# Performance work log

Hardware: AMD Instinct MI355X
Metric: run time of the kernel (lower is better)

## Reference

```python
import jax, jax.numpy as jnp
import numpy as np

N = 8192      # nodes
E = 131072    # global edges
SDIM = 256    # scalar channels
VDIM = 64     # vector channels
EDIM = 128    # edge feature dim
L = 5         # num_layers
DIN = 2 * SDIM + EDIM + 4        # [s_src, s_tgt, e, d, a, |p_src|, |p_tgt|]
DOUT = SDIM + 2 * VDIM + 1 + EDIM  # [m_s, w_v1, w_v2, w_p, e_new]
HID = SDIM


def setup_inputs() -> dict:
    key = jax.random.key(0)
    ks = jax.random.split(key, 12)
    s = jax.random.normal(ks[0], (N, SDIM), jnp.float32)
    v = 0.1 * jax.random.normal(ks[1], (N, 3, VDIM), jnp.float32)
    p = 3.0 * jax.random.normal(ks[2], (N, 3), jnp.float32)
    e = jax.random.normal(ks[3], (E, EDIM), jnp.float32)
    edge_index = jax.random.randint(ks[4], (2, E), 0, N, dtype=jnp.int32)
    W1 = jax.random.normal(ks[5], (L, DIN, HID), jnp.float32) / np.sqrt(DIN)
    W2 = jax.random.normal(ks[6], (L, HID, DOUT), jnp.float32) / np.sqrt(HID)
    U1 = jax.random.normal(ks[7], (L, SDIM, SDIM), jnp.float32) / np.sqrt(SDIM)
    U2 = jax.random.normal(ks[8], (L, SDIM, SDIM), jnp.float32) / np.sqrt(SDIM)
    return {
        's': s, 'v': v, 'p': p, 'e': e, 'edge_index': edge_index,
        'ln_g': jnp.ones((L, SDIM), jnp.float32),
        'ln_b': jnp.zeros((L, SDIM), jnp.float32),
        'W1': W1, 'b1': jnp.zeros((L, HID), jnp.float32),
        'W2': W2, 'b2': jnp.zeros((L, DOUT), jnp.float32),
        'U1': U1, 'bU1': jnp.zeros((L, SDIM), jnp.float32),
        'U2': U2, 'bU2': jnp.zeros((L, SDIM), jnp.float32),
    }


def _edge_attrs(edge_index, pos):
    # Faithful to calculate_edge_attrs (sqrt=True, no ligand-pocket branch)
    src, tgt = edge_index[0], edge_index[1]
    r = pos[tgt] - pos[src]                                   # [E,3]
    a = jnp.sum(pos[tgt] * pos[src], axis=-1)                 # [E]
    d = jnp.sqrt(jnp.clip(jnp.sum(r * r, axis=-1), 1e-6, None))
    r_norm = r / (1.0 + d[:, None])
    return d, a, r_norm


def reference(s, v, p, e, edge_index, ln_g, ln_b, W1, b1, W2, b2, U1, bU1, U2, bU2):
    src, tgt = edge_index[0], edge_index[1]
    d, a, rn = _edge_attrs(edge_index, p)
    # in-degree counts for 'mean' vector/position aggregation
    cnt = jnp.clip(jax.ops.segment_sum(jnp.ones((E,), s.dtype), tgt, num_segments=N), 1.0)
    for i in range(L):
        # LayerNorm on scalar channels (vectors passed through)
        mu = jnp.mean(s, axis=-1, keepdims=True)
        var = jnp.mean((s - mu) ** 2, axis=-1, keepdims=True)
        s_ln = ln_g[i] * (s - mu) * jax.lax.rsqrt(var + 1e-5) + ln_b[i]
        pn = jnp.linalg.norm(p, axis=-1, keepdims=True)       # use_pos_norm features
        # gather-compute edge messages
        feat = jnp.concatenate(
            [s_ln[src], s_ln[tgt], e, d[:, None], a[:, None], pn[src], pn[tgt]], axis=-1)
        h = jax.nn.silu(feat @ W1[i] + b1[i])                 # [E,HID]
        out = h @ W2[i] + b2[i]                               # [E,DOUT]
        m_s = out[:, :SDIM]
        wv1 = out[:, SDIM:SDIM + VDIM]
        wv2 = out[:, SDIM + VDIM:SDIM + 2 * VDIM]
        wp = out[:, SDIM + 2 * VDIM:SDIM + 2 * VDIM + 1]
        e_new = out[:, SDIM + 2 * VDIM + 1:]
        has_v = 0.0 if i == 0 else 1.0                        # has_v_in = (i > 0)
        m_v = has_v * wv1[:, None, :] * v[src] + wv2[:, None, :] * rn[:, :, None]  # [E,3,VDIM]
        m_p = jnp.tanh(wp) * rn                               # [E,3]
        # scatter-aggregate (sum for scalars, mean for vectors/positions)
        s = s + jax.ops.segment_sum(m_s, tgt, num_segments=N)
        v = v + jax.ops.segment_sum(m_v, tgt, num_segments=N) / cnt[:, None, None]
        p = p + jax.ops.segment_sum(m_p, tgt, num_segments=N) / cnt[:, None]
        if i < L - 1:                                         # use_mlp_update = (i < num_layers - 1)
            s = s + jax.nn.silu(s @ U1[i] + bU1[i]) @ U2[i] + bU2[i]
        e = jax.nn.silu(e_new)
        # recompute_edge_attributes=True: redo gather/distance math on new positions
        d, a, rn = _edge_attrs(edge_index, p)
    return s, v, e, p
```

## Files before the change

### kernel.cpp

```cpp
#include <hip/hip_runtime.h>
#include <hip/hip_bf16.h>

namespace {

constexpr int NN   = 8192;
constexpr int NE   = 131072;
constexpr int SD   = 256;
constexpr int ED   = 128;
constexpr int NL   = 5;
constexpr int DINc = 644;
constexpr int KE   = 160;
constexpr int TE   = 5;
constexpr int T2   = 8;
constexpr int DOUTc= 513;
constexpr int HIDc = 256;

typedef __bf16 bf16x8 __attribute__((ext_vector_type(8)));
typedef float  f32x4  __attribute__((ext_vector_type(4)));

__device__ __forceinline__ float siluf(float x) { return x / (1.0f + __expf(-x)); }

__device__ __forceinline__ void gl_lds16(const void* gsrc, void* lds_uniform_base) {
  __builtin_amdgcn_global_load_lds(
      (const __attribute__((address_space(1))) unsigned int*)gsrc,
      (__attribute__((address_space(3))) unsigned int*)lds_uniform_base, 16, 0, 0);
}

__device__ __forceinline__ void wait_vm4() {
  asm volatile("s_waitcnt vmcnt(4)" ::: "memory");
  __builtin_amdgcn_sched_barrier(0);
}
__device__ __forceinline__ void wait_vm0() {
  asm volatile("s_waitcnt vmcnt(0)" ::: "memory");
  __builtin_amdgcn_sched_barrier(0);
}

__device__ __host__ __forceinline__ int swz(int kc) { return (kc * 5) & 7; }
__device__ __forceinline__ int apos(int kc, int row) { return kc * 64  + (row ^ swz(kc)); }
__device__ __forceinline__ int bpos(int kc, int n)   { return kc * 256 + (n   ^ swz(kc)); }

enum { MODE_LIN = 4 };
enum { SRC_BF16 = 1, SRC_F32 = 2 };

struct GemmArgs {
  const __hip_bfloat16* Wt;
  const float* bias;
  const __hip_bfloat16* Abf;
  const float* Af32;
  __hip_bfloat16* bf_out;
  const __hip_bfloat16* Wtb;
  const float* biasb;
  __hip_bfloat16* bf_outb;
  int dual;
};

__device__ __forceinline__ uint4 cvt8f(const float* p) {
  alignas(16) __hip_bfloat16 t8[8];
#pragma unroll
  for (int i = 0; i < 8; i++) t8[i] = __float2bfloat16(p[i]);
  return *(const uint4*)t8;
}

template<int MODE, int SRC, int KTOT, int BM>
__global__ __launch_bounds__(256) void gemm_k(GemmArgs g) {
  constexpr int T = KTOT / 32;
  constexpr int NC = KTOT / 8;
  constexpr int RPT = 256 / BM;
  constexpr int RMASK = RPT - 1;
  __shared__ alignas(16) unsigned short Apan[NC * BM * 8];
  __shared__ alignas(16) unsigned short Bsh[2][4 * 256 * 8];
  const int tid = threadIdx.x, lane = tid & 63, wave = tid >> 6;
  const int l16 = lane & 15, lhi = lane >> 4;
  const __hip_bfloat16* wtp = g.Wt;
  const float* biasp = g.bias;
  __hip_bfloat16* outp = g.bf_out;
  int blk = blockIdx.x;
  {
    const int half = gridDim.x >> 1;
    if (g.dual && blk >= half) { blk -= half; wtp = g.Wtb; biasp = g.biasb; outp = g.bf_outb; }
  }
  const int row0 = blk * BM;
  const int ar = tid / RPT, aq = tid % RPT;
  const int arow = row0 + ar;
  f32x4 acc[BM / 16][4] = {};

  auto issueB = [&](int t, int buf) {
    const __hip_bfloat16* src = wtp + (size_t)t * 1024 * 8;
    unsigned short* dst = &Bsh[buf][0];
#pragma unroll
    for (int i = 0; i < 4; i++)
      gl_lds16(src + (size_t)(i * 256 + wave * 64 + lane) * 8, dst + (i * 256 + wave * 64) * 8);
  };

  issueB(0, 0);
#pragma unroll
  for (int j = 0; j < NC / RPT; j++) {
    const int c = j * RPT + aq;
    uint4 o;
    if constexpr (SRC == SRC_BF16) o = *(const uint4*)(g.Abf + (size_t)arow * KTOT + c * 8);
    else                           o = cvt8f(g.Af32 + (size_t)arow * KTOT + c * 8);
    *(uint4*)&Apan[(c * BM + (ar ^ swz(aq))) * 8] = o;
  }
  __syncthreads();

  int cur = 0;
  for (int t = 0; t < T; ++t) {
    if (t + 1 < T) { issueB(t + 1, cur ^ 1); wait_vm4(); }
    else           { wait_vm0(); }
    bf16x8 bfr[4];
#pragma unroll
    for (int f = 0; f < 4; f++)
      bfr[f] = *(const bf16x8*)&Bsh[cur][bpos(lhi, wave * 64 + f * 16 + l16) * 8];
#pragma unroll
    for (int fr = 0; fr < BM / 16; fr++) {
      const int kc = t * 4 + lhi;
      const bf16x8 afr = *(const bf16x8*)&Apan[(kc * BM + ((fr * 16 + l16) ^ swz(kc & RMASK))) * 8];
#pragma unroll
      for (int fc = 0; fc < 4; fc++)
        acc[fr][fc] = __builtin_amdgcn_mfma_f32_16x16x32_bf16(afr, bfr[fc], acc[fr][fc], 0, 0, 0);
    }
    cur ^= 1;
  }

#pragma unroll
  for (int fr = 0; fr < BM / 16; fr++) {
#pragma unroll
    for (int fc = 0; fc < 4; fc++) {
      const int n = wave * 64 + fc * 16 + l16;
#pragma unroll
      for (int r = 0; r < 4; r++) {
        const int row = row0 + fr * 16 + lhi * 4 + r;
        outp[(size_t)row * HIDc + n] = __float2bfloat16(acc[fr][fc][r] + biasp[n]);
      }
    }
  }
}

struct Node3Args {
  const __hip_bfloat16* W2a;
  const __hip_bfloat16* U1s;
  const __hip_bfloat16* U2s;
  const float* b2L;
  const float* bU1;
  const float* bU2;
  const float* Hagg;
  const int* rawcnt;
  float* s_out;
};

template<int LAST>
__global__ __launch_bounds__(256) void node3_k(Node3Args g) {
  constexpr int BM = 32, RPT = 8, NC = 32, T = 8;
  __shared__ alignas(16) unsigned short Apan[NC * BM * 8];
  __shared__ alignas(16) unsigned short Bsh[2][4 * 256 * 8];
  const int tid = threadIdx.x, lane = tid & 63, wave = tid >> 6;
  const int l16 = lane & 15, lhi = lane >> 4;
  const int row0 = blockIdx.x * BM;
  const int ar = tid >> 3, aq = tid & 7;

  auto issueB = [&](const __hip_bfloat16* W, int t, int buf) {
    const __hip_bfloat16* src = W + (size_t)t * 1024 * 8;
    unsigned short* dst = &Bsh[buf][0];
#pragma unroll
    for (int i = 0; i < 4; i++)
      gl_lds16(src + (size_t)(i * 256 + wave * 64 + lane) * 8, dst + (i * 256 + wave * 64) * 8);
  };

  f32x4 acc[4][2];
  auto kloop = [&](const __hip_bfloat16* W) {
#pragma unroll
    for (int i = 0; i < 4; i++)
#pragma unroll
      for (int j = 0; j < 2; j++) acc[i][j] = f32x4{0.f, 0.f, 0.f, 0.f};
    int cur = 0;
    for (int t = 0; t < T; ++t) {
      if (t + 1 < T) { issueB(W, t + 1, cur ^ 1); wait_vm4(); }
      else           { wait_vm0(); }
      bf16x8 wfr[4], afr[2];
#pragma unroll
      for (int f = 0; f < 4; f++)
        wfr[f] = *(const bf16x8*)&Bsh[cur][bpos(lhi, wave * 64 + f * 16 + l16) * 8];
#pragma unroll
      for (int f = 0; f < 2; f++) {
        const int kc = t * 4 + lhi;
        afr[f] = *(const bf16x8*)&Apan[(kc * BM + ((f * 16 + l16) ^ swz(kc & 7))) * 8];
      }
#pragma unroll
      for (int fr = 0; fr < 4; fr++)
#pragma unroll
        for (int fc = 0; fc < 2; fc++)
          acc[fr][fc] = __builtin_amdgcn_mfma_f32_16x16x32_bf16(wfr[fr], afr[fc], acc[fr][fc], 0, 0, 0);
      cur ^= 1;
    }
  };

  issueB(g.W2a, 0, 0);
#pragma unroll
  for (int j = 0; j < NC / RPT; j++) {
    const int c = j * RPT + aq;
    uint4 o = cvt8f(g.Hagg + (size_t)(row0 + ar) * SD + c * 8);
    *(uint4*)&Apan[(c * BM + (ar ^ swz(aq))) * 8] = o;
  }
  __syncthreads();

  kloop(g.W2a);
  __syncthreads();
  if constexpr (!LAST) issueB(g.U1s, 0, 0);

#pragma unroll
  for (int fr = 0; fr < 4; fr++) {
    const int nb = wave * 64 + fr * 16 + lhi * 4;
    const int kc = nb >> 3, off = nb & 7;
    const f32x4 b4 = *(const f32x4*)(g.b2L + nb);
#pragma unroll
    for (int fc = 0; fc < 2; fc++) {
      const int row = fc * 16 + l16;
      const float rc = (float)g.rawcnt[row0 + row];
      float* sp = g.s_out + (size_t)(row0 + row) * SD + nb;
      f32x4 sold = *(const f32x4*)sp;
      alignas(8) __hip_bfloat16 hb[4];
      f32x4 s1;
#pragma unroll
      for (int r = 0; r < 4; r++) {
        s1[r] = sold[r] + acc[fr][fc][r] + rc * b4[r];
        hb[r] = __float2bfloat16(s1[r]);
      }
      *(f32x4*)sp = s1;
      if constexpr (!LAST)
        *(uint2*)&Apan[(kc * BM + (row ^ swz(kc & 7))) * 8 + off] = *(const uint2*)hb;
    }
  }
  if constexpr (LAST) return;

  __syncthreads();

  kloop(g.U1s);
  __syncthreads();
  issueB(g.U2s, 0, 0);
#pragma unroll
  for (int fr = 0; fr < 4; fr++) {
    const int nb = wave * 64 + fr * 16 + lhi * 4;
    const int kc = nb >> 3, off = nb & 7;
    const f32x4 b4 = *(const f32x4*)(g.bU1 + nb);
#pragma unroll
    for (int fc = 0; fc < 2; fc++) {
      const int row = fc * 16 + l16;
      alignas(8) __hip_bfloat16 hb[4];
#pragma unroll
      for (int r = 0; r < 4; r++)
        hb[r] = __float2bfloat16(siluf(acc[fr][fc][r] + b4[r]));
      *(uint2*)&Apan[(kc * BM + (row ^ swz(kc & 7))) * 8 + off] = *(const uint2*)hb;
    }
  }
  __syncthreads();

  kloop(g.U2s);
#pragma unroll
  for (int fr = 0; fr < 4; fr++) {
    const int nb = wave * 64 + fr * 16 + lhi * 4;
    const f32x4 b4 = *(const f32x4*)(g.bU2 + nb);
#pragma unroll
    for (int fc = 0; fc < 2; fc++) {
      const int row = fc * 16 + l16;
      float* sp = g.s_out + (size_t)(row0 + row) * SD + nb;
      f32x4 s1 = *(const f32x4*)sp;
#pragma unroll
      for (int r = 0; r < 4; r++) s1[r] += acc[fr][fc][r] + b4[r];
      *(f32x4*)sp = s1;
    }
  }
}

struct FusedArgs {
  const __hip_bfloat16* W1e;
  const __hip_bfloat16* W2s;
  const float* b2L;
  const int* src; const int* tgt;
  const int* rank;
  const __hip_bfloat16* e_bf;
  const __hip_bfloat16* tail;
  const __hip_bfloat16* p1;
  const __hip_bfloat16* p2;
  const __hip_bfloat16* w384;
  const float* rn;
  float* mp;
  __hip_bfloat16* h_out;
  __hip_bfloat16* wv_out;
  __hip_bfloat16* e_bf_out;
  float* e_f32_out;
  int write_e_f32;
};

__global__ __launch_bounds__(256) void fused_k(FusedArgs g) {
  __shared__ alignas(16) unsigned short Ash[4 * 64 * 8];
  __shared__ alignas(16) unsigned short Bsh[2][4 * 256 * 8];
  __shared__ alignas(16) unsigned short Hsh[32 * 64 * 8];
  __shared__ float wps[4][64];
  __shared__ int Rk[64];
  const int tid = threadIdx.x, lane = tid & 63, wave = tid >> 6;
  const int l16 = lane & 15, lhi = lane >> 4;
  const int row0 = blockIdx.x * 64;
  const int ar = tid >> 2, aq = tid & 3;
  const int arow = row0 + ar;
  const int sn = g.src[arow], tn = g.tgt[arow];

  auto issueW = [&](const __hip_bfloat16* W, int t, int buf) {
    const __hip_bfloat16* src = W + (size_t)t * 1024 * 8;
    unsigned short* dst = &Bsh[buf][0];
#pragma unroll
    for (int i = 0; i < 4; i++)
      gl_lds16(src + (size_t)(i * 256 + wave * 64 + lane) * 8, dst + (i * 256 + wave * 64) * 8);
  };
  auto loadA = [&](int t, uint4& o) {
    const int kq = t * 32 + aq * 8;
    if (kq < 128) o = *(const uint4*)(g.e_bf + (size_t)arow * ED + kq);
    else          o = *(const uint4*)(g.tail + (size_t)arow * 32 + (kq - 128));
  };

  uint4 a;
  loadA(0, a);
  issueW(g.W1e, 0, 0);
  if (tid < 64) Rk[tid] = g.rank[row0 + tid];

#pragma unroll
  for (int j = 0; j < 8; j++) {
    const int c = j * 4 + aq;
    uint4 r1 = *(const uint4*)(g.p1 + (size_t)sn * SD + c * 8);
    uint4 r2 = *(const uint4*)(g.p2 + (size_t)tn * SD + c * 8);
    const __hip_bfloat16* h1 = (const __hip_bfloat16*)&r1;
    const __hip_bfloat16* h2 = (const __hip_bfloat16*)&r2;
    alignas(16) __hip_bfloat16 o8[8];
#pragma unroll
    for (int m = 0; m < 8; m++)
      o8[m] = __float2bfloat16(__bfloat162float(h1[m]) + __bfloat162float(h2[m]));
    *(uint4*)&Hsh[(c * 64 + (ar ^ swz(aq))) * 8] = *(const uint4*)o8;
  }

  f32x4 acc1[4][4] = {};
  int cur = 0;
  for (int t = 0; t < TE; ++t) {
    *(uint4*)&Ash[apos(aq, ar) * 8] = a;
    __syncthreads();
    if (t + 1 < TE) { issueW(g.W1e, t + 1, cur ^ 1); loadA(t + 1, a); }
    bf16x8 wfr[4], efr[4];
#pragma unroll
    for (int f = 0; f < 4; f++) {
      wfr[f] = *(const bf16x8*)&Bsh[cur][bpos(lhi, wave * 64 + f * 16 + l16) * 8];
      efr[f] = *(const bf16x8*)&Ash[apos(lhi, f * 16 + l16) * 8];
    }
#pragma unroll
    for (int fr = 0; fr < 4; fr++)
#pragma unroll
      for (int fc = 0; fc < 4; fc++)
        acc1[fr][fc] = __builtin_amdgcn_mfma_f32_16x16x32_bf16(wfr[fr], efr[fc], acc1[fr][fc], 0, 0, 0);
    __syncthreads();
    cur ^= 1;
  }

  issueW(g.W2s, 0, 0);

  float pw[4] = {0.f, 0.f, 0.f, 0.f};
#pragma unroll
  for (int fr = 0; fr < 4; fr++) {
    const int nb = wave * 64 + fr * 16 + lhi * 4;
    const int kc = nb >> 3, off = nb & 7;
    uint2 wr = *(const uint2*)(g.w384 + nb);
    const __hip_bfloat16* w4 = (const __hip_bfloat16*)&wr;
#pragma unroll
    for (int fc = 0; fc < 4; fc++) {
      const int row = fc * 16 + l16;
      unsigned short* slot = &Hsh[(kc * 64 + (row ^ swz(kc & 3))) * 8 + off];
      uint2 pr = *(const uint2*)slot;
      const __hip_bfloat16* pp = (const __hip_bfloat16*)&pr;
      alignas(8) __hip_bfloat16 hb[4];
#pragma unroll
      for (int r = 0; r < 4; r++) {
        const float hv = siluf(acc1[fr][fc][r] + __bfloat162float(pp[r]));
        hb[r] = __float2bfloat16(hv);
        pw[fc] += hv * __bfloat162float(w4[r]);
      }
      *(uint2*)slot = *(const uint2*)hb;
      *(uint2*)(g.h_out + (size_t)Rk[row] * HIDc + nb) = *(const uint2*)hb;
    }
  }

#pragma unroll
  for (int fc = 0; fc < 4; fc++) {
    pw[fc] += __shfl_xor(pw[fc], 16);
    pw[fc] += __shfl_xor(pw[fc], 32);
  }
  if (lane < 16) {
#pragma unroll
    for (int fc = 0; fc < 4; fc++) wps[wave][fc * 16 + lane] = pw[fc];
  }
  __syncthreads();
  if (tid < 64) {
    const float s = wps[0][tid] + wps[1][tid] + wps[2][tid] + wps[3][tid];
    const float wpt = tanhf(s + g.b2L[384]);
    const int rk = Rk[tid];
#pragma unroll
    for (int c = 0; c < 3; c++)
      g.mp[(size_t)rk * 3 + c] = wpt * g.rn[(size_t)(row0 + tid) * 3 + c];
  }

  f32x4 acc2[4][4] = {};
  cur = 0;
  for (int t = 0; t < T2; ++t) {
    if (t + 1 < T2) { issueW(g.W2s, t + 1, cur ^ 1); wait_vm4(); }
    else            { wait_vm0(); }
    bf16x8 afr[4], bfr[4];
#pragma unroll
    for (int f = 0; f < 4; f++) {
      const int kc = t * 4 + lhi;
      afr[f] = *(const bf16x8*)&Hsh[(kc * 64 + ((f * 16 + l16) ^ swz(lhi))) * 8];
      bfr[f] = *(const bf16x8*)&Bsh[cur][bpos(lhi, wave * 64 + f * 16 + l16) * 8];
    }
#pragma unroll
    for (int fr = 0; fr < 4; fr++)
#pragma unroll
      for (int fc = 0; fc < 4; fc++)
        acc2[fr][fc] = __builtin_amdgcn_mfma_f32_16x16x32_bf16(afr[fr], bfr[fc], acc2[fr][fc], 0, 0, 0);
    cur ^= 1;
  }

#pragma unroll
  for (int fr = 0; fr < 4; fr++) {
#pragma unroll
    for (int fc = 0; fc < 4; fc++) {
      const int n = wave * 64 + fc * 16 + l16;
#pragma unroll
      for (int r = 0; r < 4; r++) {
        const int lr = fr * 16 + lhi * 4 + r;
        const int row = row0 + lr;
        const float valf = acc2[fr][fc][r];
        if (n < 128) {
          g.wv_out[(size_t)Rk[lr] * 128 + n] = __float2bfloat16(valf + g.b2L[256 + n]);
        } else {
          const float sv = siluf(valf + g.b2L[257 + n]);
          g.e_bf_out[(size_t)row * ED + (n - 128)] = __float2bfloat16(sv);
          if (g.write_e_f32) g.e_f32_out[(size_t)row * ED + (n - 128)] = sv;
        }
      }
    }
  }
}

__global__ __launch_bounds__(256) void ln_k(const float* __restrict__ s,
                                            const float* __restrict__ gl, const float* __restrict__ bl,
                                            __hip_bfloat16* __restrict__ s_ln) {
  const int wave = threadIdx.x >> 6, lane = threadIdx.x & 63;
  const int node = blockIdx.x * 4 + wave;
  const float* srow = s + (size_t)node * SD;
  float x[4], sum = 0.f, sq = 0.f;
#pragma unroll
  for (int i = 0; i < 4; i++) { x[i] = srow[lane * 4 + i]; sum += x[i]; sq += x[i] * x[i]; }
#pragma unroll
  for (int off = 1; off < 64; off <<= 1) { sum += __shfl_xor(sum, off); sq += __shfl_xor(sq, off); }
  const float mu = sum * (1.0f / SD);
  const float var = sq * (1.0f / SD) - mu * mu;
  const float rstd = rsqrtf(var + 1e-5f);
#pragma unroll
  for (int i = 0; i < 4; i++) {
    const int c = lane * 4 + i;
    s_ln[(size_t)node * SD + c] = __float2bfloat16(gl[c] * (x[i] - mu) * rstd + bl[c]);
  }
}

__global__ void edge_attr_k(const float* __restrict__ p, const int* __restrict__ src, const int* __restrict__ tgt,
                            const int* __restrict__ rank,
                            float* __restrict__ rn, float* __restrict__ rnp,
                            __hip_bfloat16* __restrict__ tail) {
  const int e = blockIdx.x * blockDim.x + threadIdx.x;
  if (e >= NE) return;
  const int s_ = src[e], t_ = tgt[e];
  const float sx = p[s_ * 3], sy = p[s_ * 3 + 1], sz = p[s_ * 3 + 2];
  const float tx = p[t_ * 3], ty = p[t_ * 3 + 1], tz = p[t_ * 3 + 2];
  const float rx = tx - sx, ry = ty - sy, rz = tz - sz;
  const float a = tx * sx + ty * sy + tz * sz;
  const float rr = rx * rx + ry * ry + rz * rz;
  const float d = sqrtf(fmaxf(rr, 1e-6f));
  const float inv = 1.0f / (1.0f + d);
  const float r0 = rx * inv, r1 = ry * inv, r2 = rz * inv;
  rn[e * 3] = r0; rn[e * 3 + 1] = r1; rn[e * 3 + 2] = r2;
  const int rk = rank[e];
  rnp[rk * 3] = r0; rnp[rk * 3 + 1] = r1; rnp[rk * 3 + 2] = r2;
  alignas(16) __hip_bfloat16 t8[8];
  t8[0] = __float2bfloat16(d);
  t8[1] = __float2bfloat16(a);
  t8[2] = __float2bfloat16(sqrtf(sx * sx + sy * sy + sz * sz));
  t8[3] = __float2bfloat16(sqrtf(tx * tx + ty * ty + tz * tz));
  t8[4] = t8[5] = t8[6] = t8[7] = __float2bfloat16(0.0f);
  __hip_bfloat16* tp = tail + (size_t)e * 32;
  uint4 z; z.x = z.y = z.z = z.w = 0;
  *(uint4*)tp = *(const uint4*)t8;
  *(uint4*)(tp + 8) = z;
  *(uint4*)(tp + 16) = z;
  *(uint4*)(tp + 24) = z;
}

__global__ void cvt_e_k(const float* __restrict__ e, __hip_bfloat16* __restrict__ ebf) {
  const int i = blockIdx.x * blockDim.x + threadIdx.x;
  const float* p = e + (size_t)i * 8;
  alignas(16) __hip_bfloat16 t8[8];
#pragma unroll
  for (int j = 0; j < 8; j++) t8[j] = __float2bfloat16(p[j]);
  *(uint4*)(ebf + (size_t)i * 8) = *(const uint4*)t8;
}

__global__ void count_k(const int* __restrict__ tgt, int* __restrict__ rawcnt) {
  const int e = blockIdx.x * blockDim.x + threadIdx.x;
  if (e < NE) atomicAdd(&rawcnt[tgt[e]], 1);
}

__global__ __launch_bounds__(256) void scan_k(const int* __restrict__ rawcnt, int* __restrict__ off) {
  __shared__ int ts[256];
  const int tid = threadIdx.x;
  const int base = tid * 32;
  int local[32];
  int s = 0;
#pragma unroll
  for (int i = 0; i < 32; i++) { local[i] = s; s += rawcnt[base + i]; }
  ts[tid] = s;
  __syncthreads();
  if (tid == 0) {
    int acc = 0;
    for (int i = 0; i < 256; i++) { int t = ts[i]; ts[i] = acc; acc += t; }
    off[NN] = acc;
  }
  __syncthreads();
  const int pre = ts[tid];
#pragma unroll
  for (int i = 0; i < 32; i++) off[base + i] = pre + local[i];
}

__global__ void scatter_k(const int* __restrict__ tgt, const int* __restrict__ srcp,
                          const int* __restrict__ off,
                          int* __restrict__ cursor, int* __restrict__ rank, int* __restrict__ psrc) {
  const int e = blockIdx.x * blockDim.x + threadIdx.x;
  if (e < NE) {
    const int t = tgt[e];
    const int pos = off[t] + atomicAdd(&cursor[t], 1);
    rank[e] = pos;
    psrc[pos] = srcp[e];
  }
}

__global__ __launch_bounds__(256) void agg_k(const int* __restrict__ off, const int* __restrict__ psrc,
                                             const __hip_bfloat16* __restrict__ h,
                                             const __hip_bfloat16* __restrict__ wv,
                                             const float* __restrict__ mp,
                                             const float* __restrict__ rnp,
                                             const float* __restrict__ v_old,
                                             float* __restrict__ v_new,
                                             float* __restrict__ Hagg,
                                             float* __restrict__ p_o,
                                             int hasv) {
  const int n = blockIdx.x;
  const int c = threadIdx.x;
  const int e0 = off[n], e1 = off[n + 1];
  const int c3 = c >> 6, ln = c & 63;
  float hs = 0.f, vs = 0.f, ps = 0.f;
  int j = e0;
  for (; j + 2 <= e1; j += 2) {
    const float h0 = __bfloat162float(h[(size_t)j * HIDc + c]);
    const float h1 = __bfloat162float(h[(size_t)(j + 1) * HIDc + c]);
    hs += h0 + h1;
    if (c < 192) {
      const int s0 = psrc[j], s1 = psrc[j + 1];
      float m0 = __bfloat162float(wv[(size_t)j * 128 + 64 + ln]) * rnp[j * 3 + c3];
      float m1 = __bfloat162float(wv[(size_t)(j + 1) * 128 + 64 + ln]) * rnp[(j + 1) * 3 + c3];
      if (hasv) {
        m0 += __bfloat162float(wv[(size_t)j * 128 + ln]) * v_old[(size_t)s0 * 192 + c];
        m1 += __bfloat162float(wv[(size_t)(j + 1) * 128 + ln]) * v_old[(size_t)s1 * 192 + c];
      }
      vs += m0 + m1;
    } else if (c < 195) {
      ps += mp[j * 3 + (c - 192)] + mp[(j + 1) * 3 + (c - 192)];
    }
  }
  for (; j < e1; j++) {
    hs += __bfloat162float(h[(size_t)j * HIDc + c]);
    if (c < 192) {
      float mv = __bfloat162float(wv[(size_t)j * 128 + 64 + ln]) * rnp[j * 3 + c3];
      if (hasv) mv += __bfloat162float(wv[(size_t)j * 128 + ln]) * v_old[(size_t)psrc[j] * 192 + c];
      vs += mv;
    } else if (c < 195) {
      ps += mp[j * 3 + (c - 192)];
    }
  }
  Hagg[(size_t)n * HIDc + c] = hs;
  const float inv = 1.0f / fmaxf((float)(e1 - e0), 1.0f);
  if (c < 192)      v_new[(size_t)n * 192 + c] = v_old[(size_t)n * 192 + c] + vs * inv;
  else if (c < 195) p_o[n * 3 + (c - 192)]    += ps * inv;
}

__global__ void zero_k(float* __restrict__ ptr, int n) {
  const int i = blockIdx.x * blockDim.x + threadIdx.x;
  if (i < n) ptr[i] = 0.f;
}

__global__ void prep_w1abs_k(const float* __restrict__ W1, __hip_bfloat16* __restrict__ W1aS,
                             __hip_bfloat16* __restrict__ W1bS) {
  const int idx = blockIdx.x * blockDim.x + threadIdx.x;
  if (idx >= NL * T2 * 1024) return;
  const int p = idx & 1023, t = (idx >> 10) % T2, l = idx / (T2 * 1024);
  const int kc = p >> 8, n = (p & 255) ^ swz(kc);
  alignas(16) __hip_bfloat16 a8[8], b8[8];
#pragma unroll
  for (int j = 0; j < 8; j++) {
    const int k = t * 32 + kc * 8 + j;
    a8[j] = __float2bfloat16(W1[((size_t)l * DINc + k) * HIDc + n]);
    b8[j] = __float2bfloat16(W1[((size_t)l * DINc + 256 + k) * HIDc + n]);
  }
  *(uint4*)(W1aS + (size_t)idx * 8) = *(const uint4*)a8;
  *(uint4*)(W1bS + (size_t)idx * 8) = *(const uint4*)b8;
}

__global__ void prep_w1es_k(const float* __restrict__ W1, __hip_bfloat16* __restrict__ W1eS) {
  const int idx = blockIdx.x * blockDim.x + threadIdx.x;
  if (idx >= NL * TE * 1024) return;
  const int p = idx & 1023, t = (idx >> 10) % TE, l = idx / (TE * 1024);
  const int kc = p >> 8, n = (p & 255) ^ swz(kc);
  alignas(16) __hip_bfloat16 e8[8];
#pragma unroll
  for (int j = 0; j < 8; j++) {
    const int k = t * 32 + kc * 8 + j;
    const int row = (k < 128) ? (512 + k) : ((k < 132) ? (640 + (k - 128)) : -1);
    e8[j] = __float2bfloat16(row >= 0 ? W1[((size_t)l * DINc + row) * HIDc + n] : 0.f);
  }
  *(uint4*)(W1eS + (size_t)idx * 8) = *(const uint4*)e8;
}

__global__ void prep_w2s_k(const float* __restrict__ W2, __hip_bfloat16* __restrict__ W2sS,
                           __hip_bfloat16* __restrict__ W2aS) {
  const int idx = blockIdx.x * blockDim.x + threadIdx.x;
  if (idx >= NL * T2 * 1024) return;
  const int p = idx & 1023, t = (idx >> 10) & 7, l = idx >> 13;
  const int kc = p >> 8, n = (p & 255) ^ swz(kc);
  const float* W2l = W2 + (size_t)l * HIDc * DOUTc;
  const int cs = (n < 128) ? (256 + n) : (257 + n);
  alignas(16) __hip_bfloat16 s8[8], a8[8];
#pragma unroll
  for (int j = 0; j < 8; j++) {
    const int k = t * 32 + kc * 8 + j;
    s8[j] = __float2bfloat16(W2l[(size_t)k * DOUTc + cs]);
    a8[j] = __float2bfloat16(W2l[(size_t)k * DOUTc + n]);
  }
  *(uint4*)(W2sS + (size_t)idx * 8) = *(const uint4*)s8;
  *(uint4*)(W2aS + (size_t)idx * 8) = *(const uint4*)a8;
}

__global__ void prep_uts_k(const float* __restrict__ U1, const float* __restrict__ U2,
                           __hip_bfloat16* __restrict__ U1S, __hip_bfloat16* __restrict__ U2S) {
  const int idx = blockIdx.x * blockDim.x + threadIdx.x;
  if (idx >= NL * T2 * 1024) return;
  const int p = idx & 1023, t = (idx >> 10) & 7, l = idx >> 13;
  const int kc = p >> 8, n = (p & 255) ^ swz(kc);
  alignas(16) __hip_bfloat16 u1[8], u2[8];
#pragma unroll
  for (int j = 0; j < 8; j++) {
    const int k = t * 32 + kc * 8 + j;
    u1[j] = __float2bfloat16(U1[((size_t)l * HIDc + k) * HIDc + n]);
    u2[j] = __float2bfloat16(U2[((size_t)l * HIDc + k) * HIDc + n]);
  }
  *(uint4*)(U1S + (size_t)idx * 8) = *(const uint4*)u1;
  *(uint4*)(U2S + (size_t)idx * 8) = *(const uint4*)u2;
}

__global__ void prep_w384_k(const float* __restrict__ W2, __hip_bfloat16* __restrict__ w384) {
  const int idx = blockIdx.x * blockDim.x + threadIdx.x;
  if (idx >= NL * HIDc) return;
  const int k = idx & 255, l = idx >> 8;
  w384[idx] = __float2bfloat16(W2[((size_t)l * HIDc + k) * DOUTc + 384]);
}

}

extern "C" void kernel_launch(void* const* d_in, const int* in_sizes, int n_in,
                              void* d_out, int out_size, void* d_ws, size_t ws_size,
                              hipStream_t stream) {
  (void)in_sizes; (void)n_in; (void)out_size; (void)ws_size;
  const float* s_in = (const float*)d_in[0];
  const float* v_in = (const float*)d_in[1];
  const float* p_in = (const float*)d_in[2];
  const float* e_in = (const float*)d_in[3];
  const int*   ei   = (const int*)d_in[4];
  const float* ln_g = (const float*)d_in[5];
  const float* ln_b = (const float*)d_in[6];
  const float* W1   = (const float*)d_in[7];
  const float* b1   = (const float*)d_in[8];
  const float* W2   = (const float*)d_in[9];
  const float* b2   = (const float*)d_in[10];
  const float* U1   = (const float*)d_in[11];
  const float* bU1  = (const float*)d_in[12];
  const float* U2   = (const float*)d_in[13];
  const float* bU2  = (const float*)d_in[14];

  float* s_o = (float*)d_out;
  float* v_o = s_o + (size_t)NN * SD;
  float* e_o = v_o + (size_t)NN * 192;
  float* p_o = e_o + (size_t)NE * ED;

  const int* srcp = ei;
  const int* tgtp = ei + NE;

  char* wp = (char*)d_ws;
  auto alloc = [&](size_t bytes) -> char* {
    char* r = wp; wp += (bytes + 255) & ~(size_t)255; return r;
  };
  __hip_bfloat16* s_ln = (__hip_bfloat16*)alloc((size_t)NN * SD * 2);
  __hip_bfloat16* hbuf = (__hip_bfloat16*)alloc((size_t)NE * HIDc * 2);
  __hip_bfloat16* ebf  = (__hip_bfloat16*)alloc((size_t)NE * ED * 2);
  __hip_bfloat16* wvbuf= (__hip_bfloat16*)alloc((size_t)NE * 128 * 2);
  __hip_bfloat16* tailb= (__hip_bfloat16*)alloc((size_t)NE * 32 * 2);
  __hip_bfloat16* p1buf= (__hip_bfloat16*)alloc((size_t)NN * SD * 2);
  __hip_bfloat16* p2buf= (__hip_bfloat16*)alloc((size_t)NN * SD * 2);
  float* rnbuf = (float*)alloc((size_t)NE * 3 * 4);
  float* rnpbuf= (float*)alloc((size_t)NE * 3 * 4);
  float* Hagg  = (float*)alloc((size_t)NN * SD * 4);
  float* vprev = (float*)alloc((size_t)NN * 192 * 4);
  float* mpbuf = (float*)alloc((size_t)NE * 3 * 4);
  float* zerobias = (float*)alloc(256 * 4);
  int*   rawcnt= (int*)alloc((size_t)NN * 4);
  int*   offb  = (int*)alloc((size_t)(NN + 1) * 4);
  int*   cursor= (int*)alloc((size_t)NN * 4);
  int*   rankb = (int*)alloc((size_t)NE * 4);
  int*   psrcb = (int*)alloc((size_t)NE * 4);
  __hip_bfloat16* W1aS = (__hip_bfloat16*)alloc((size_t)NL * T2 * 1024 * 8 * 2);
  __hip_bfloat16* W1bS = (__hip_bfloat16*)alloc((size_t)NL * T2 * 1024 * 8 * 2);
  __hip_bfloat16* W1eS = (__hip_bfloat16*)alloc((size_t)NL * TE * 1024 * 8 * 2);
  __hip_bfloat16* W2sS = (__hip_bfloat16*)alloc((size_t)NL * T2 * 1024 * 8 * 2);
  __hip_bfloat16* W2aS = (__hip_bfloat16*)alloc((size_t)NL * T2 * 1024 * 8 * 2);
  __hip_bfloat16* U1S  = (__hip_bfloat16*)alloc((size_t)NL * T2 * 1024 * 8 * 2);
  __hip_bfloat16* U2S  = (__hip_bfloat16*)alloc((size_t)NL * T2 * 1024 * 8 * 2);
  __hip_bfloat16* w384 = (__hip_bfloat16*)alloc((size_t)NL * HIDc * 2);

  hipMemcpyAsync(s_o, s_in, (size_t)NN * SD * 4, hipMemcpyDeviceToDevice, stream);
  hipMemcpyAsync(vprev, v_in, (size_t)NN * 192 * 4, hipMemcpyDeviceToDevice, stream);
  hipMemcpyAsync(p_o, p_in, (size_t)NN * 3 * 4, hipMemcpyDeviceToDevice, stream);

  prep_w1abs_k<<<(NL * T2 * 1024 + 255) / 256, 256, 0, stream>>>(W1, W1aS, W1bS);
  prep_w1es_k<<<(NL * TE * 1024 + 255) / 256, 256, 0, stream>>>(W1, W1eS);
  prep_w2s_k<<<(NL * T2 * 1024 + 255) / 256, 256, 0, stream>>>(W2, W2sS, W2aS);
  prep_uts_k<<<(NL * T2 * 1024 + 255) / 256, 256, 0, stream>>>(U1, U2, U1S, U2S);
  prep_w384_k<<<(NL * HIDc + 255) / 256, 256, 0, stream>>>(W2, w384);
  cvt_e_k<<<NE * ED / 8 / 256, 256, 0, stream>>>(e_in, ebf);
  zero_k<<<1, 256, 0, stream>>>(zerobias, 256);

  zero_k<<<(NN + 255) / 256, 256, 0, stream>>>((float*)rawcnt, NN);
  zero_k<<<(NN + 255) / 256, 256, 0, stream>>>((float*)cursor, NN);
  count_k<<<NE / 256, 256, 0, stream>>>(tgtp, rawcnt);
  scan_k<<<1, 256, 0, stream>>>(rawcnt, offb);
  scatter_k<<<NE / 256, 256, 0, stream>>>(tgtp, srcp, offb, cursor, rankb, psrcb);

  for (int l = 0; l < NL; l++) {
    ln_k<<<NN / 4, 256, 0, stream>>>(s_o, ln_g + l * SD, ln_b + l * SD, s_ln);
    edge_attr_k<<<NE / 256, 256, 0, stream>>>(p_o, srcp, tgtp, rankb, rnbuf, rnpbuf, tailb);

    GemmArgs gp{};
    gp.Wt = W1aS + (size_t)l * T2 * 1024 * 8; gp.bias = b1 + l * HIDc; gp.bf_out = p1buf;
    gp.Wtb = W1bS + (size_t)l * T2 * 1024 * 8; gp.biasb = zerobias; gp.bf_outb = p2buf;
    gp.Abf = s_ln; gp.dual = 1;
    gemm_k<MODE_LIN, SRC_BF16, 256, 64><<<2 * NN / 64, 256, 0, stream>>>(gp);

    FusedArgs gf{};
    gf.W1e = W1eS + (size_t)l * TE * 1024 * 8;
    gf.W2s = W2sS + (size_t)l * T2 * 1024 * 8;
    gf.b2L = b2 + l * DOUTc;
    gf.src = srcp; gf.tgt = tgtp; gf.rank = rankb;
    gf.e_bf = ebf; gf.tail = tailb;
    gf.p1 = p1buf; gf.p2 = p2buf; gf.w384 = w384 + l * HIDc;
    gf.rn = rnbuf; gf.mp = mpbuf;
    gf.h_out = hbuf; gf.wv_out = wvbuf; gf.e_bf_out = ebf; gf.e_f32_out = e_o;
    gf.write_e_f32 = (l == NL - 1) ? 1 : 0;
    fused_k<<<NE / 64, 256, 0, stream>>>(gf);

    const float* vold = (l & 1) ? (const float*)v_o : (const float*)vprev;
    float* vnew = (l & 1) ? vprev : v_o;
    agg_k<<<NN, 256, 0, stream>>>(offb, psrcb, hbuf, wvbuf, mpbuf, rnpbuf,
                                  vold, vnew, Hagg, p_o, (l > 0) ? 1 : 0);

    Node3Args gn{};
    gn.W2a = W2aS + (size_t)l * T2 * 1024 * 8;
    gn.U1s = U1S + (size_t)l * T2 * 1024 * 8;
    gn.U2s = U2S + (size_t)l * T2 * 1024 * 8;
    gn.b2L = b2 + l * DOUTc; gn.bU1 = bU1 + l * HIDc; gn.bU2 = bU2 + l * HIDc;
    gn.Hagg = Hagg; gn.rawcnt = rawcnt; gn.s_out = s_o;
    if (l < NL - 1) node3_k<0><<<NN / 32, 256, 0, stream>>>(gn);
    else            node3_k<1><<<NN / 32, 256, 0, stream>>>(gn);
  }
}
```

Measured before the change: 1.092 ms.

## Fuse next-layer LayerNorm and W1 node projections into node update; inline edge attrs

The node-update kernel now applies the next layer's LayerNorm to the updated scalars in its epilogue, using a block-level mean/variance reduction. It then runs the two W1 node-projection GEMMs (p1/p2) in place, so the separate ln_k and dual gemm_k launches drop out of every layer after the first. Edge attributes (r_norm, distance, dot product, norms) are computed inside fused_k from positions and kept in LDS. This removes the edge_attr_k launch and the rn and tail buffers it wrote and re-read. In exchange, node3_k does more serial work per block on a small grid, and the edge-attribute gathers now sit in the fused kernel's prologue.

```diff
diff --git a/kernel.cpp b/kernel.cpp
--- a/kernel.cpp
+++ b/kernel.cpp
@@ -39,14 +39,12 @@
 __device__ __forceinline__ int apos(int kc, int row) { return kc * 64  + (row ^ swz(kc)); }
 __device__ __forceinline__ int bpos(int kc, int n)   { return kc * 256 + (n   ^ swz(kc)); }
 
-enum { MODE_LIN = 4 };
-enum { SRC_BF16 = 1, SRC_F32 = 2 };
+enum { SRC_BF16 = 1 };
 
 struct GemmArgs {
   const __hip_bfloat16* Wt;
   const float* bias;
   const __hip_bfloat16* Abf;
-  const float* Af32;
   __hip_bfloat16* bf_out;
   const __hip_bfloat16* Wtb;
   const float* biasb;
@@ -61,7 +59,7 @@
   return *(const uint4*)t8;
 }
 
-template<int MODE, int SRC, int KTOT, int BM>
+template<int KTOT, int BM>
 __global__ __launch_bounds__(256) void gemm_k(GemmArgs g) {
   constexpr int T = KTOT / 32;
   constexpr int NC = KTOT / 8;
@@ -96,9 +94,7 @@
 #pragma unroll
   for (int j = 0; j < NC / RPT; j++) {
     const int c = j * RPT + aq;
-    uint4 o;
-    if constexpr (SRC == SRC_BF16) o = *(const uint4*)(g.Abf + (size_t)arow * KTOT + c * 8);
-    else                           o = cvt8f(g.Af32 + (size_t)arow * KTOT + c * 8);
+    uint4 o = *(const uint4*)(g.Abf + (size_t)arow * KTOT + c * 8);
     *(uint4*)&Apan[(c * BM + (ar ^ swz(aq))) * 8] = o;
   }
   __syncthreads();
@@ -140,12 +136,19 @@
   const __hip_bfloat16* W2a;
   const __hip_bfloat16* U1s;
   const __hip_bfloat16* U2s;
+  const __hip_bfloat16* W1an;
+  const __hip_bfloat16* W1bn;
   const float* b2L;
   const float* bU1;
   const float* bU2;
+  const float* b1n;
+  const float* lng;
+  const float* lnb;
   const float* Hagg;
   const int* rawcnt;
   float* s_out;
+  __hip_bfloat16* p1;
+  __hip_bfloat16* p2;
 };
 
 template<int LAST>
@@ -153,6 +156,7 @@
   constexpr int BM = 32, RPT = 8, NC = 32, T = 8;
   __shared__ alignas(16) unsigned short Apan[NC * BM * 8];
   __shared__ alignas(16) unsigned short Bsh[2][4 * 256 * 8];
+  __shared__ float red[2][4][32];
   const int tid = threadIdx.x, lane = tid & 63, wave = tid >> 6;
   const int l16 = lane & 15, lhi = lane >> 4;
   const int row0 = blockIdx.x * BM;
@@ -255,6 +259,7 @@
   __syncthreads();
 
   kloop(g.U2s);
+  float psum[2] = {0.f, 0.f}, psq[2] = {0.f, 0.f};
 #pragma unroll
   for (int fr = 0; fr < 4; fr++) {
     const int nb = wave * 64 + fr * 16 + lhi * 4;
@@ -263,10 +268,85 @@
     for (int fc = 0; fc < 2; fc++) {
       const int row = fc * 16 + l16;
       float* sp = g.s_out + (size_t)(row0 + row) * SD + nb;
-      f32x4 s1 = *(const f32x4*)sp;
-#pragma unroll
-      for (int r = 0; r < 4; r++) s1[r] += acc[fr][fc][r] + b4[r];
-      *(f32x4*)sp = s1;
+      f32x4 sv = *(const f32x4*)sp;
+#pragma unroll
+      for (int r = 0; r < 4; r++) {
+        sv[r] += acc[fr][fc][r] + b4[r];
+        psum[fc] += sv[r];
+        psq[fc] += sv[r] * sv[r];
+      }
+      *(f32x4*)sp = sv;
+      acc[fr][fc] = sv;
+    }
+  }
+#pragma unroll
+  for (int fc = 0; fc < 2; fc++) {
+    psum[fc] += __shfl_xor(psum[fc], 16); psum[fc] += __shfl_xor(psum[fc], 32);
+    psq[fc]  += __shfl_xor(psq[fc], 16);  psq[fc]  += __shfl_xor(psq[fc], 32);
+  }
+  if (lane < 16) {
+    red[0][wave][lane] = psum[0]; red[0][wave][16 + lane] = psum[1];
+    red[1][wave][lane] = psq[0];  red[1][wave][16 + lane] = psq[1];
+  }
+  __syncthreads();
+
+  float mu2[2], rs2[2];
+#pragma unroll
+  for (int fc = 0; fc < 2; fc++) {
+    const int ri = fc * 16 + l16;
+    const float S = red[0][0][ri] + red[0][1][ri] + red[0][2][ri] + red[0][3][ri];
+    const float Q = red[1][0][ri] + red[1][1][ri] + red[1][2][ri] + red[1][3][ri];
+    const float mu = S * (1.0f / SD);
+    const float var = Q * (1.0f / SD) - mu * mu;
+    mu2[fc] = mu; rs2[fc] = rsqrtf(var + 1e-5f);
+  }
+#pragma unroll
+  for (int fr = 0; fr < 4; fr++) {
+    const int nb = wave * 64 + fr * 16 + lhi * 4;
+    const int kc = nb >> 3, off = nb & 7;
+    const f32x4 g4 = *(const f32x4*)(g.lng + nb);
+    const f32x4 bb4 = *(const f32x4*)(g.lnb + nb);
+#pragma unroll
+    for (int fc = 0; fc < 2; fc++) {
+      const int row = fc * 16 + l16;
+      alignas(8) __hip_bfloat16 hb[4];
+#pragma unroll
+      for (int r = 0; r < 4; r++)
+        hb[r] = __float2bfloat16(g4[r] * (acc[fr][fc][r] - mu2[fc]) * rs2[fc] + bb4[r]);
+      *(uint2*)&Apan[(kc * BM + (row ^ swz(kc & 7))) * 8 + off] = *(const uint2*)hb;
+    }
+  }
+  issueB(g.W1an, 0, 0);
+  __syncthreads();
+
+  kloop(g.W1an);
+#pragma unroll
+  for (int fr = 0; fr < 4; fr++) {
+    const int nb = wave * 64 + fr * 16 + lhi * 4;
+    const f32x4 b4 = *(const f32x4*)(g.b1n + nb);
+#pragma unroll
+    for (int fc = 0; fc < 2; fc++) {
+      const int row = fc * 16 + l16;
+      alignas(8) __hip_bfloat16 hb[4];
+#pragma unroll
+      for (int r = 0; r < 4; r++)
+        hb[r] = __float2bfloat16(acc[fr][fc][r] + b4[r]);
+      *(uint2*)(g.p1 + (size_t)(row0 + row) * SD + nb) = *(const uint2*)hb;
+    }
+  }
+  issueB(g.W1bn, 0, 0);
+  kloop(g.W1bn);
+#pragma unroll
+  for (int fr = 0; fr < 4; fr++) {
+    const int nb = wave * 64 + fr * 16 + lhi * 4;
+#pragma unroll
+    for (int fc = 0; fc < 2; fc++) {
+      const int row = fc * 16 + l16;
+      alignas(8) __hip_bfloat16 hb[4];
+#pragma unroll
+      for (int r = 0; r < 4; r++)
+        hb[r] = __float2bfloat16(acc[fr][fc][r]);
+      *(uint2*)(g.p2 + (size_t)(row0 + row) * SD + nb) = *(const uint2*)hb;
     }
   }
 }
@@ -277,12 +357,12 @@
   const float* b2L;
   const int* src; const int* tgt;
   const int* rank;
+  const float* pos;
   const __hip_bfloat16* e_bf;
-  const __hip_bfloat16* tail;
   const __hip_bfloat16* p1;
   const __hip_bfloat16* p2;
   const __hip_bfloat16* w384;
-  const float* rn;
+  float* rnp;
   float* mp;
   __hip_bfloat16* h_out;
   __hip_bfloat16* wv_out;
@@ -296,6 +376,8 @@
   __shared__ alignas(16) unsigned short Bsh[2][4 * 256 * 8];
   __shared__ alignas(16) unsigned short Hsh[32 * 64 * 8];
   __shared__ float wps[4][64];
+  __shared__ float RnL[64][3];
+  __shared__ unsigned int EdL[64][2];
   __shared__ int Rk[64];
   const int tid = threadIdx.x, lane = tid & 63, wave = tid >> 6;
   const int l16 = lane & 15, lhi = lane >> 4;
@@ -312,15 +394,41 @@
       gl_lds16(src + (size_t)(i * 256 + wave * 64 + lane) * 8, dst + (i * 256 + wave * 64) * 8);
   };
   auto loadA = [&](int t, uint4& o) {
-    const int kq = t * 32 + aq * 8;
-    if (kq < 128) o = *(const uint4*)(g.e_bf + (size_t)arow * ED + kq);
-    else          o = *(const uint4*)(g.tail + (size_t)arow * 32 + (kq - 128));
+    if (t < 4) {
+      o = *(const uint4*)(g.e_bf + (size_t)arow * ED + t * 32 + aq * 8);
+    } else {
+      o.x = o.y = o.z = o.w = 0;
+      if (aq == 0) { o.x = EdL[ar][0]; o.y = EdL[ar][1]; }
+    }
   };
 
   uint4 a;
   loadA(0, a);
   issueW(g.W1e, 0, 0);
-  if (tid < 64) Rk[tid] = g.rank[row0 + tid];
+
+  if (tid < 64) {
+    const int e = row0 + tid;
+    const int rk = g.rank[e];
+    Rk[tid] = rk;
+    const int s_ = g.src[e], t_ = g.tgt[e];
+    const float sx = g.pos[s_ * 3], sy = g.pos[s_ * 3 + 1], sz = g.pos[s_ * 3 + 2];
+    const float tx = g.pos[t_ * 3], ty = g.pos[t_ * 3 + 1], tz = g.pos[t_ * 3 + 2];
+    const float rx = tx - sx, ry = ty - sy, rz = tz - sz;
+    const float av = tx * sx + ty * sy + tz * sz;
+    const float rr = rx * rx + ry * ry + rz * rz;
+    const float d = sqrtf(fmaxf(rr, 1e-6f));
+    const float inv = 1.0f / (1.0f + d);
+    const float r0 = rx * inv, r1 = ry * inv, r2 = rz * inv;
+    RnL[tid][0] = r0; RnL[tid][1] = r1; RnL[tid][2] = r2;
+    g.rnp[rk * 3] = r0; g.rnp[rk * 3 + 1] = r1; g.rnp[rk * 3 + 2] = r2;
+    alignas(8) __hip_bfloat16 q[4];
+    q[0] = __float2bfloat16(d);
+    q[1] = __float2bfloat16(av);
+    q[2] = __float2bfloat16(sqrtf(sx * sx + sy * sy + sz * sz));
+    q[3] = __float2bfloat16(sqrtf(tx * tx + ty * ty + tz * tz));
+    EdL[tid][0] = ((const unsigned*)q)[0];
+    EdL[tid][1] = ((const unsigned*)q)[1];
+  }
 
 #pragma unroll
   for (int j = 0; j < 8; j++) {
@@ -400,7 +508,7 @@
     const int rk = Rk[tid];
 #pragma unroll
     for (int c = 0; c < 3; c++)
-      g.mp[(size_t)rk * 3 + c] = wpt * g.rn[(size_t)(row0 + tid) * 3 + c];
+      g.mp[(size_t)rk * 3 + c] = wpt * RnL[tid][c];
   }
 
   f32x4 acc2[4][4] = {};
@@ -464,38 +572,6 @@
     const int c = lane * 4 + i;
     s_ln[(size_t)node * SD + c] = __float2bfloat16(gl[c] * (x[i] - mu) * rstd + bl[c]);
   }
-}
-
-__global__ void edge_attr_k(const float* __restrict__ p, const int* __restrict__ src, const int* __restrict__ tgt,
-                            const int* __restrict__ rank,
-                            float* __restrict__ rn, float* __restrict__ rnp,
-                            __hip_bfloat16* __restrict__ tail) {
-  const int e = blockIdx.x * blockDim.x + threadIdx.x;
-  if (e >= NE) return;
-  const int s_ = src[e], t_ = tgt[e];
-  const float sx = p[s_ * 3], sy = p[s_ * 3 + 1], sz = p[s_ * 3 + 2];
-  const float tx = p[t_ * 3], ty = p[t_ * 3 + 1], tz = p[t_ * 3 + 2];
-  const float rx = tx - sx, ry = ty - sy, rz = tz - sz;
-  const float a = tx * sx + ty * sy + tz * sz;
-  const float rr = rx * rx + ry * ry + rz * rz;
-  const float d = sqrtf(fmaxf(rr, 1e-6f));
-  const float inv = 1.0f / (1.0f + d);
-  const float r0 = rx * inv, r1 = ry * inv, r2 = rz * inv;
-  rn[e * 3] = r0; rn[e * 3 + 1] = r1; rn[e * 3 + 2] = r2;
-  const int rk = rank[e];
-  rnp[rk * 3] = r0; rnp[rk * 3 + 1] = r1; rnp[rk * 3 + 2] = r2;
-  alignas(16) __hip_bfloat16 t8[8];
-  t8[0] = __float2bfloat16(d);
-  t8[1] = __float2bfloat16(a);
-  t8[2] = __float2bfloat16(sqrtf(sx * sx + sy * sy + sz * sz));
-  t8[3] = __float2bfloat16(sqrtf(tx * tx + ty * ty + tz * tz));
-  t8[4] = t8[5] = t8[6] = t8[7] = __float2bfloat16(0.0f);
-  __hip_bfloat16* tp = tail + (size_t)e * 32;
-  uint4 z; z.x = z.y = z.z = z.w = 0;
-  *(uint4*)tp = *(const uint4*)t8;
-  *(uint4*)(tp + 8) = z;
-  *(uint4*)(tp + 16) = z;
-  *(uint4*)(tp + 24) = z;
 }
 
 __global__ void cvt_e_k(const float* __restrict__ e, __hip_bfloat16* __restrict__ ebf) {
@@ -712,10 +788,8 @@
   __hip_bfloat16* hbuf = (__hip_bfloat16*)alloc((size_t)NE * HIDc * 2);
   __hip_bfloat16* ebf  = (__hip_bfloat16*)alloc((size_t)NE * ED * 2);
   __hip_bfloat16* wvbuf= (__hip_bfloat16*)alloc((size_t)NE * 128 * 2);
-  __hip_bfloat16* tailb= (__hip_bfloat16*)alloc((size_t)NE * 32 * 2);
   __hip_bfloat16* p1buf= (__hip_bfloat16*)alloc((size_t)NN * SD * 2);
   __hip_bfloat16* p2buf= (__hip_bfloat16*)alloc((size_t)NN * SD * 2);
-  float* rnbuf = (float*)alloc((size_t)NE * 3 * 4);
   float* rnpbuf= (float*)alloc((size_t)NE * 3 * 4);
   float* Hagg  = (float*)alloc((size_t)NN * SD * 4);
   float* vprev = (float*)alloc((size_t)NN * 192 * 4);
@@ -753,24 +827,22 @@
   scan_k<<<1, 256, 0, stream>>>(rawcnt, offb);
   scatter_k<<<NE / 256, 256, 0, stream>>>(tgtp, srcp, offb, cursor, rankb, psrcb);
 
+  ln_k<<<NN / 4, 256, 0, stream>>>(s_o, ln_g, ln_b, s_ln);
+  GemmArgs gp{};
+  gp.Wt = W1aS; gp.bias = b1; gp.bf_out = p1buf;
+  gp.Wtb = W1bS; gp.biasb = zerobias; gp.bf_outb = p2buf;
+  gp.Abf = s_ln; gp.dual = 1;
+  gemm_k<256, 64><<<2 * NN / 64, 256, 0, stream>>>(gp);
+
   for (int l = 0; l < NL; l++) {
-    ln_k<<<NN / 4, 256, 0, stream>>>(s_o, ln_g + l * SD, ln_b + l * SD, s_ln);
-    edge_attr_k<<<NE / 256, 256, 0, stream>>>(p_o, srcp, tgtp, rankb, rnbuf, rnpbuf, tailb);
-
-    GemmArgs gp{};
-    gp.Wt = W1aS + (size_t)l * T2 * 1024 * 8; gp.bias = b1 + l * HIDc; gp.bf_out = p1buf;
-    gp.Wtb = W1bS + (size_t)l * T2 * 1024 * 8; gp.biasb = zerobias; gp.bf_outb = p2buf;
-    gp.Abf = s_ln; gp.dual = 1;
-    gemm_k<MODE_LIN, SRC_BF16, 256, 64><<<2 * NN / 64, 256, 0, stream>>>(gp);
-
     FusedArgs gf{};
     gf.W1e = W1eS + (size_t)l * TE * 1024 * 8;
     gf.W2s = W2sS + (size_t)l * T2 * 1024 * 8;
     gf.b2L = b2 + l * DOUTc;
     gf.src = srcp; gf.tgt = tgtp; gf.rank = rankb;
-    gf.e_bf = ebf; gf.tail = tailb;
+    gf.pos = p_o; gf.e_bf = ebf;
     gf.p1 = p1buf; gf.p2 = p2buf; gf.w384 = w384 + l * HIDc;
-    gf.rn = rnbuf; gf.mp = mpbuf;
+    gf.rnp = rnpbuf; gf.mp = mpbuf;
     gf.h_out = hbuf; gf.wv_out = wvbuf; gf.e_bf_out = ebf; gf.e_f32_out = e_o;
     gf.write_e_f32 = (l == NL - 1) ? 1 : 0;
     fused_k<<<NE / 64, 256, 0, stream>>>(gf);
@@ -786,7 +858,15 @@
     gn.U2s = U2S + (size_t)l * T2 * 1024 * 8;
     gn.b2L = b2 + l * DOUTc; gn.bU1 = bU1 + l * HIDc; gn.bU2 = bU2 + l * HIDc;
     gn.Hagg = Hagg; gn.rawcnt = rawcnt; gn.s_out = s_o;
-    if (l < NL - 1) node3_k<0><<<NN / 32, 256, 0, stream>>>(gn);
-    else            node3_k<1><<<NN / 32, 256, 0, stream>>>(gn);
-  }
-}
+    if (l < NL - 1) {
+      gn.W1an = W1aS + (size_t)(l + 1) * T2 * 1024 * 8;
+      gn.W1bn = W1bS + (size_t)(l + 1) * T2 * 1024 * 8;
+      gn.b1n = b1 + (l + 1) * HIDc;
+      gn.lng = ln_g + (l + 1) * SD; gn.lnb = ln_b + (l + 1) * SD;
+      gn.p1 = p1buf; gn.p2 = p2buf;
+      node3_k<0><<<NN / 32, 256, 0, stream>>>(gn);
+    } else {
+      node3_k<1><<<NN / 32, 256, 0, stream>>>(gn);
+    }
+  }
+}
```

New measurement: 1.020 ms, median of 2. -6.6%, faster.
